# Kernel tuning notes

Hardware: AMD Instinct MI355X
Metric: run time of the kernel (lower is better)

## Reference

```python
import jax, jax.numpy as jnp
import numpy as np

N_NODES = 50000
N_EDGES = 800000
C_IN = 128
C_OUT = 64
C_HID = 2 * C_OUT  # 128


def setup_inputs() -> dict:
    key = jax.random.key(0)
    ks = jax.random.split(key, 8)
    x = jax.random.normal(ks[0], (N_NODES, C_IN), dtype=jnp.float32)
    edge_index = jax.random.randint(ks[1], (2, N_EDGES), 0, N_NODES, dtype=jnp.int64)
    s1 = 1.0 / np.sqrt(C_IN)
    s2 = 1.0 / np.sqrt(C_HID)
    s3 = 1.0 / np.sqrt(C_OUT)
    W1 = jax.random.uniform(ks[2], (C_IN, C_HID), jnp.float32, -s1, s1)
    b1 = jnp.zeros((C_HID,), jnp.float32)
    W2 = jax.random.uniform(ks[3], (C_HID, C_OUT), jnp.float32, -s2, s2)
    b2 = jnp.zeros((C_OUT,), jnp.float32)
    Wb = jax.random.uniform(ks[4], (1, C_OUT, C_OUT), jnp.float32, -s3, s3)
    bb = jax.random.uniform(ks[5], (1,), jnp.float32, -s3, s3)
    return {"x": x, "edge_index": edge_index, "W1": W1, "b1": b1,
            "W2": W2, "b2": b2, "Wb": Wb, "bb": bb}


def gcn_conv(x, W, b, src, dst, n_nodes):
    # PyG GCNConv: h = x @ W; add self-loops; symmetric normalization D^-1/2 (A+I) D^-1/2.
    h = x @ W  # [N, F]
    ones = jnp.ones((src.shape[0],), h.dtype)
    deg = jax.ops.segment_sum(ones, dst, num_segments=n_nodes) + 1.0  # +1 for self-loop
    dinv = jax.lax.rsqrt(deg)
    norm = dinv[src] * dinv[dst]  # [E]
    msgs = h[src] * norm[:, None]  # [E, F]
    agg = jax.ops.segment_sum(msgs, dst, num_segments=n_nodes)
    # self-loop contribution: norm_ii = 1/deg_i
    agg = agg + h * (1.0 / deg)[:, None]
    return agg + b


def reference(x, edge_index, W1, b1, W2, b2, Wb, bb):
    src = edge_index[0]
    dst = edge_index[1]
    n = x.shape[0]
    # encode
    h = jax.nn.relu(gcn_conv(x, W1, b1, src, dst, n))
    z = gcn_conv(h, W2, b2, src, dst, n)  # [N, C_OUT]
    # decode: bilinear on (z[src], z[dst]) -> sigmoid
    zs = z[src]  # [E, C_OUT]
    zd = z[dst]  # [E, C_OUT]
    logits = jnp.einsum('ec,ocd,ed->eo', zs, Wb, zd) + bb  # [E, 1]
    return jax.nn.sigmoid(logits)
```

## Files before the change

kernel.cpp:

```cpp
#include <hip/hip_runtime.h>
#include <hip/hip_bf16.h>


#define N_NODES 50000
#define BSH 7
#define BSZ 128
#define NBUCK ((N_NODES + BSZ - 1) / BSZ)
#define EPB 4096
#define CAP 3072
#define DSPLIT 4

typedef unsigned int u32;
typedef unsigned short u16;
typedef unsigned long long u64;

typedef __attribute__((ext_vector_type(8))) short bf16x8;
typedef __attribute__((ext_vector_type(4))) float f32x4;
union frag_u { bf16x8 f; u32 u[4]; uint4 v; };

__device__ __forceinline__ float bflo(u32 u) { return __uint_as_float(u << 16); }
__device__ __forceinline__ float bfhi(u32 u) { return __uint_as_float(u & 0xffff0000u); }
__device__ __forceinline__ u32 f2bf(float f) {
    u32 b = __float_as_uint(f);
    return (b + 0x7fffu + ((b >> 16) & 1u)) >> 16;
}
__device__ __forceinline__ u32 pack2(float a, float b) { return f2bf(a) | (f2bf(b) << 16); }

__global__ __launch_bounds__(256) void gemm1_scatter(
        const float* __restrict__ X, const float* __restrict__ W,
        u16* __restrict__ O, int n_rows, int gblk,
        const int* __restrict__ src, const int* __restrict__ dst,
        int* __restrict__ bcur, u64* __restrict__ pair, int E) {
    constexpr int K = 128, NOUT = 128;
    constexpr int KP = K + 8;
    constexpr int NT = NOUT / 16;
    constexpr int KS = K / 32;
    __shared__ __align__(16) char smem[NOUT * KP * 2 * sizeof(u16)];
    int t = threadIdx.x;

    if ((int)blockIdx.x < gblk) {
        u16* Wt_hi = (u16*)smem;
        u16* Wt_lo = Wt_hi + NOUT * KP;
        for (int i4 = t; i4 < K * NOUT / 4; i4 += 256) {
            int k = (i4 * 4) / NOUT;
            int n0 = (i4 * 4) % NOUT;
            float4 w4 = *(const float4*)&W[(size_t)k * NOUT + n0];
            float wv[4] = {w4.x, w4.y, w4.z, w4.w};
#pragma unroll
            for (int q = 0; q < 4; q++) {
                u32 hi = f2bf(wv[q]);
                u32 lo = f2bf(wv[q] - bflo(hi));
                Wt_hi[(n0 + q) * KP + k] = (u16)hi;
                Wt_lo[(n0 + q) * KP + k] = (u16)lo;
            }
        }
        __syncthreads();

        int wave = t >> 6;
        int lane = t & 63;
        int m16 = lane & 15;
        int quad = lane >> 4;
        int row0 = blockIdx.x * 128 + wave * 32;

        f32x4 acc[2][NT] = {};
        for (int ks = 0; ks < KS; ks++) {
            frag_u a_hi[2], a_lo[2];
#pragma unroll
            for (int mt = 0; mt < 2; mt++) {
                int row = row0 + mt * 16 + m16;
                row = row < n_rows ? row : n_rows - 1;
                const float* Xp = X + (size_t)row * K + ks * 32 + quad * 8;
                float4 x0 = *(const float4*)Xp;
                float4 x1 = *(const float4*)(Xp + 4);
                float xv[8] = {x0.x, x0.y, x0.z, x0.w, x1.x, x1.y, x1.z, x1.w};
#pragma unroll
                for (int p = 0; p < 4; p++) {
                    u32 h0 = f2bf(xv[2 * p]), h1 = f2bf(xv[2 * p + 1]);
                    a_hi[mt].u[p] = h0 | (h1 << 16);
                    a_lo[mt].u[p] = pack2(xv[2 * p] - bflo(h0), xv[2 * p + 1] - bflo(h1));
                }
            }
#pragma unroll
            for (int nt = 0; nt < NT; nt++) {
                int n = nt * 16 + m16;
                frag_u b_hi, b_lo;
                b_hi.v = *(const uint4*)&Wt_hi[n * KP + ks * 32 + quad * 8];
                b_lo.v = *(const uint4*)&Wt_lo[n * KP + ks * 32 + quad * 8];
#pragma unroll
                for (int mt = 0; mt < 2; mt++) {
                    acc[mt][nt] = __builtin_amdgcn_mfma_f32_16x16x32_bf16(a_hi[mt].f, b_hi.f, acc[mt][nt], 0, 0, 0);
                    acc[mt][nt] = __builtin_amdgcn_mfma_f32_16x16x32_bf16(a_hi[mt].f, b_lo.f, acc[mt][nt], 0, 0, 0);
                    acc[mt][nt] = __builtin_amdgcn_mfma_f32_16x16x32_bf16(a_lo[mt].f, b_hi.f, acc[mt][nt], 0, 0, 0);
                }
            }
        }
#pragma unroll
        for (int mt = 0; mt < 2; mt++)
#pragma unroll
            for (int nt = 0; nt < NT; nt++)
#pragma unroll
                for (int r = 0; r < 4; r++) {
                    int row = row0 + mt * 16 + quad * 4 + r;
                    if (row < n_rows)
                        O[(size_t)row * NOUT + nt * 16 + m16] = (u16)f2bf(acc[mt][nt][r]);
                }
    } else {
        int* hist = (int*)smem;
        for (int i = t; i < NBUCK; i += 256) hist[i] = 0;
        __syncthreads();
        int base = ((int)blockIdx.x - gblk) * EPB;
        int s_[16], d_[16];
#pragma unroll
        for (int it = 0; it < 16; it++) {
            int e = base + it * 256 + t;
            if (e < E) {
                s_[it] = src[e];
                d_[it] = dst[e];
                atomicAdd(&hist[d_[it] >> BSH], 1);
            } else {
                d_[it] = -1;
            }
        }
        __syncthreads();
        for (int b = t; b < NBUCK; b += 256) {
            int c = hist[b];
            hist[b] = c ? (b * CAP + atomicAdd(&bcur[b], c)) : 0;
        }
        __syncthreads();
#pragma unroll
        for (int it = 0; it < 16; it++) {
            if (d_[it] >= 0) {
                int b = d_[it] >> BSH;
                int off = atomicAdd(&hist[b], 1);
                int e = base + it * 256 + t;
                pair[off] = (u64)((u32)s_[it] | ((u32)(d_[it] & (BSZ - 1)) << 16))
                          | ((u64)(u32)e << 32);
            }
        }
    }
}

__global__ __launch_bounds__(256) void bucket_sort(const u64* __restrict__ pair,
                                                   const int* __restrict__ bcur,
                                                   int* __restrict__ row_ptr,
                                                   int* __restrict__ col,
                                                   float* __restrict__ dinv,
                                                   float* __restrict__ inv, int n, int E) {
    __shared__ int ssum[256];
    __shared__ int cnt[BSZ];
    __shared__ int scn[BSZ];
    __shared__ int cur[BSZ];
    int t = threadIdx.x;
    int base = blockIdx.x << BSH;
    int nn = min(BSZ, n - base);
    int accp = 0;
    for (int i = t; i < (int)blockIdx.x; i += 256) accp += bcur[i];
    ssum[t] = accp;
    __syncthreads();
    for (int s = 128; s > 0; s >>= 1) {
        if (t < s) ssum[t] += ssum[t + s];
        __syncthreads();
    }
    int b0 = ssum[0];
    int cntE = bcur[blockIdx.x];
    int p0 = blockIdx.x * CAP;
    if (t < BSZ) cnt[t] = 0;
    __syncthreads();
    for (int j = t; j < cntE; j += 256)
        atomicAdd(&cnt[(int)((pair[p0 + j] >> 16) & (BSZ - 1))], 1);
    __syncthreads();
    if (t < BSZ) scn[t] = cnt[t];
    __syncthreads();
    for (int off = 1; off < BSZ; off <<= 1) {
        int a = (t < BSZ && t >= off) ? scn[t - off] : 0;
        __syncthreads();
        if (t < BSZ) scn[t] += a;
        __syncthreads();
    }
    if (t < nn) {
        int excl = b0 + scn[t] - cnt[t];
        row_ptr[base + t] = excl;
        cur[t] = excl;
        float d = (float)cnt[t] + 1.0f;
        dinv[base + t] = rsqrtf(d);
        inv[base + t] = 1.0f / d;
    }
    if (t == 0 && blockIdx.x == NBUCK - 1) row_ptr[n] = E;
    __syncthreads();
    for (int j = t; j < cntE; j += 256) {
        u64 p = pair[p0 + j];
        int ln = (int)((p >> 16) & (BSZ - 1));
        int pos = atomicAdd(&cur[ln], 1);
        col[pos] = (int)(p & 0xffffu);
    }
}

template <int K, int NOUT>
__global__ __launch_bounds__(256) void gemm_mfma_bf(const u16* __restrict__ Xv,
                                                    const float* __restrict__ W,
                                                    u16* __restrict__ O, int n_rows) {
    constexpr int KP = K + 8;
    constexpr int NT = NOUT / 16;
    constexpr int KS = K / 32;
    __shared__ __align__(16) u16 Wt_hi[NOUT * KP];
    __shared__ __align__(16) u16 Wt_lo[NOUT * KP];
    int t = threadIdx.x;
    for (int i4 = t; i4 < K * NOUT / 4; i4 += 256) {
        int k = (i4 * 4) / NOUT;
        int n0 = (i4 * 4) % NOUT;
        float4 w4 = *(const float4*)&W[(size_t)k * NOUT + n0];
        float wv[4] = {w4.x, w4.y, w4.z, w4.w};
#pragma unroll
        for (int q = 0; q < 4; q++) {
            u32 hi = f2bf(wv[q]);
            u32 lo = f2bf(wv[q] - bflo(hi));
            Wt_hi[(n0 + q) * KP + k] = (u16)hi;
            Wt_lo[(n0 + q) * KP + k] = (u16)lo;
        }
    }
    __syncthreads();

    int wave = t >> 6;
    int lane = t & 63;
    int m16 = lane & 15;
    int quad = lane >> 4;
    int row0 = blockIdx.x * 128 + wave * 32;

    f32x4 acc[2][NT] = {};
    for (int ks = 0; ks < KS; ks++) {
        frag_u a_hi[2];
#pragma unroll
        for (int mt = 0; mt < 2; mt++) {
            int row = row0 + mt * 16 + m16;
            row = row < n_rows ? row : n_rows - 1;
            a_hi[mt].v = *(const uint4*)(Xv + (size_t)row * K + ks * 32 + quad * 8);
        }
#pragma unroll
        for (int nt = 0; nt < NT; nt++) {
            int n = nt * 16 + m16;
            frag_u b_hi, b_lo;
            b_hi.v = *(const uint4*)&Wt_hi[n * KP + ks * 32 + quad * 8];
            b_lo.v = *(const uint4*)&Wt_lo[n * KP + ks * 32 + quad * 8];
#pragma unroll
            for (int mt = 0; mt < 2; mt++) {
                acc[mt][nt] = __builtin_amdgcn_mfma_f32_16x16x32_bf16(a_hi[mt].f, b_hi.f, acc[mt][nt], 0, 0, 0);
                acc[mt][nt] = __builtin_amdgcn_mfma_f32_16x16x32_bf16(a_hi[mt].f, b_lo.f, acc[mt][nt], 0, 0, 0);
            }
        }
    }
#pragma unroll
    for (int mt = 0; mt < 2; mt++)
#pragma unroll
        for (int nt = 0; nt < NT; nt++)
#pragma unroll
            for (int r = 0; r < 4; r++) {
                int row = row0 + mt * 16 + quad * 4 + r;
                if (row < n_rows)
                    O[(size_t)row * NOUT + nt * 16 + m16] = (u16)f2bf(acc[mt][nt][r]);
            }
}

template <int C, bool RELU>
__global__ __launch_bounds__(256) void agg_pull(const u16* __restrict__ H,
                                                const int* __restrict__ row_ptr,
                                                const int* __restrict__ col,
                                                const float* __restrict__ dinv,
                                                const float* __restrict__ inv,
                                                const float* __restrict__ b,
                                                u16* __restrict__ O, int n) {
    constexpr int TPN = C / 8;
    const uint4* Hv = (const uint4*)H;
    int tid = blockIdx.x * 256 + threadIdx.x;
    int node = tid / TPN;
    if (node >= n) return;
    int part = tid % TPN;
    int c8 = part * 8;
    float dn = dinv[node];
    float iv = inv[node];
    float acc[8];
    {
        uint4 h = Hv[(size_t)node * TPN + part];
        acc[0] = bflo(h.x) * iv + b[c8 + 0];
        acc[1] = bfhi(h.x) * iv + b[c8 + 1];
        acc[2] = bflo(h.y) * iv + b[c8 + 2];
        acc[3] = bfhi(h.y) * iv + b[c8 + 3];
        acc[4] = bflo(h.z) * iv + b[c8 + 4];
        acc[5] = bfhi(h.z) * iv + b[c8 + 5];
        acc[6] = bflo(h.w) * iv + b[c8 + 6];
        acc[7] = bfhi(h.w) * iv + b[c8 + 7];
    }
    int j = row_ptr[node];
    int end = row_ptr[node + 1];
    for (; j + 7 < end; j += 8) {
        int s0 = col[j],     s1 = col[j + 1], s2 = col[j + 2], s3 = col[j + 3];
        int s4 = col[j + 4], s5 = col[j + 5], s6 = col[j + 6], s7 = col[j + 7];
        float n0 = dn * dinv[s0], n1 = dn * dinv[s1];
        float n2 = dn * dinv[s2], n3 = dn * dinv[s3];
        float n4 = dn * dinv[s4], n5 = dn * dinv[s5];
        float n6 = dn * dinv[s6], n7 = dn * dinv[s7];
        uint4 v0 = Hv[(size_t)s0 * TPN + part];
        uint4 v1 = Hv[(size_t)s1 * TPN + part];
        uint4 v2 = Hv[(size_t)s2 * TPN + part];
        uint4 v3 = Hv[(size_t)s3 * TPN + part];
        uint4 v4 = Hv[(size_t)s4 * TPN + part];
        uint4 v5 = Hv[(size_t)s5 * TPN + part];
        uint4 v6 = Hv[(size_t)s6 * TPN + part];
        uint4 v7 = Hv[(size_t)s7 * TPN + part];
        acc[0] += bflo(v0.x) * n0 + bflo(v1.x) * n1 + bflo(v2.x) * n2 + bflo(v3.x) * n3;
        acc[1] += bfhi(v0.x) * n0 + bfhi(v1.x) * n1 + bfhi(v2.x) * n2 + bfhi(v3.x) * n3;
        acc[2] += bflo(v0.y) * n0 + bflo(v1.y) * n1 + bflo(v2.y) * n2 + bflo(v3.y) * n3;
        acc[3] += bfhi(v0.y) * n0 + bfhi(v1.y) * n1 + bfhi(v2.y) * n2 + bfhi(v3.y) * n3;
        acc[4] += bflo(v0.z) * n0 + bflo(v1.z) * n1 + bflo(v2.z) * n2 + bflo(v3.z) * n3;
        acc[5] += bfhi(v0.z) * n0 + bfhi(v1.z) * n1 + bfhi(v2.z) * n2 + bfhi(v3.z) * n3;
        acc[6] += bflo(v0.w) * n0 + bflo(v1.w) * n1 + bflo(v2.w) * n2 + bflo(v3.w) * n3;
        acc[7] += bfhi(v0.w) * n0 + bfhi(v1.w) * n1 + bfhi(v2.w) * n2 + bfhi(v3.w) * n3;
        acc[0] += bflo(v4.x) * n4 + bflo(v5.x) * n5 + bflo(v6.x) * n6 + bflo(v7.x) * n7;
        acc[1] += bfhi(v4.x) * n4 + bfhi(v5.x) * n5 + bfhi(v6.x) * n6 + bfhi(v7.x) * n7;
        acc[2] += bflo(v4.y) * n4 + bflo(v5.y) * n5 + bflo(v6.y) * n6 + bflo(v7.y) * n7;
        acc[3] += bfhi(v4.y) * n4 + bfhi(v5.y) * n5 + bfhi(v6.y) * n6 + bfhi(v7.y) * n7;
        acc[4] += bflo(v4.z) * n4 + bflo(v5.z) * n5 + bflo(v6.z) * n6 + bflo(v7.z) * n7;
        acc[5] += bfhi(v4.z) * n4 + bfhi(v5.z) * n5 + bfhi(v6.z) * n6 + bfhi(v7.z) * n7;
        acc[6] += bflo(v4.w) * n4 + bflo(v5.w) * n5 + bflo(v6.w) * n6 + bflo(v7.w) * n7;
        acc[7] += bfhi(v4.w) * n4 + bfhi(v5.w) * n5 + bfhi(v6.w) * n6 + bfhi(v7.w) * n7;
    }
    for (; j + 3 < end; j += 4) {
        int s0 = col[j], s1 = col[j + 1], s2 = col[j + 2], s3 = col[j + 3];
        float n0 = dn * dinv[s0], n1 = dn * dinv[s1];
        float n2 = dn * dinv[s2], n3 = dn * dinv[s3];
        uint4 v0 = Hv[(size_t)s0 * TPN + part];
        uint4 v1 = Hv[(size_t)s1 * TPN + part];
        uint4 v2 = Hv[(size_t)s2 * TPN + part];
        uint4 v3 = Hv[(size_t)s3 * TPN + part];
        acc[0] += bflo(v0.x) * n0 + bflo(v1.x) * n1 + bflo(v2.x) * n2 + bflo(v3.x) * n3;
        acc[1] += bfhi(v0.x) * n0 + bfhi(v1.x) * n1 + bfhi(v2.x) * n2 + bfhi(v3.x) * n3;
        acc[2] += bflo(v0.y) * n0 + bflo(v1.y) * n1 + bflo(v2.y) * n2 + bflo(v3.y) * n3;
        acc[3] += bfhi(v0.y) * n0 + bfhi(v1.y) * n1 + bfhi(v2.y) * n2 + bfhi(v3.y) * n3;
        acc[4] += bflo(v0.z) * n0 + bflo(v1.z) * n1 + bflo(v2.z) * n2 + bflo(v3.z) * n3;
        acc[5] += bfhi(v0.z) * n0 + bfhi(v1.z) * n1 + bfhi(v2.z) * n2 + bfhi(v3.z) * n3;
        acc[6] += bflo(v0.w) * n0 + bflo(v1.w) * n1 + bflo(v2.w) * n2 + bflo(v3.w) * n3;
        acc[7] += bfhi(v0.w) * n0 + bfhi(v1.w) * n1 + bfhi(v2.w) * n2 + bfhi(v3.w) * n3;
    }
    for (; j < end; j++) {
        int s = col[j];
        float nm = dn * dinv[s];
        uint4 v = Hv[(size_t)s * TPN + part];
        acc[0] += bflo(v.x) * nm; acc[1] += bfhi(v.x) * nm;
        acc[2] += bflo(v.y) * nm; acc[3] += bfhi(v.y) * nm;
        acc[4] += bflo(v.z) * nm; acc[5] += bfhi(v.z) * nm;
        acc[6] += bflo(v.w) * nm; acc[7] += bfhi(v.w) * nm;
    }
    if (RELU) {
#pragma unroll
        for (int i = 0; i < 8; i++) acc[i] = fmaxf(acc[i], 0.f);
    }
    uint4 o;
    o.x = pack2(acc[0], acc[1]);
    o.y = pack2(acc[2], acc[3]);
    o.z = pack2(acc[4], acc[5]);
    o.w = pack2(acc[6], acc[7]);
    ((uint4*)O)[(size_t)node * TPN + part] = o;
}

__global__ __launch_bounds__(256) void decode_fused(const u16* __restrict__ Z,
                                                    const float* __restrict__ Wb,
                                                    const u64* __restrict__ pair,
                                                    const int* __restrict__ bcur,
                                                    const float* __restrict__ bb,
                                                    float* __restrict__ out, int n) {
    constexpr int K = 64, NOUT = 64;
    constexpr int KP = K + 8;
    constexpr int QP = 72;
    __shared__ __align__(16) u16 Wt_hi[NOUT * KP];
    __shared__ __align__(16) u16 Wt_lo[NOUT * KP];
    __shared__ __align__(16) u16 Qs[BSZ * QP];
    int t = threadIdx.x;
    int bucket = blockIdx.x / DSPLIT;
    int part = blockIdx.x % DSPLIT;
    int base = bucket << BSH;

    for (int i4 = t; i4 < K * NOUT / 4; i4 += 256) {
        int nn_ = (i4 * 4) / K;
        int k0 = (i4 * 4) % K;
        float4 w4 = *(const float4*)&Wb[(size_t)nn_ * K + k0];
        float wv[4] = {w4.x, w4.y, w4.z, w4.w};
#pragma unroll
        for (int q = 0; q < 4; q++) {
            u32 hi = f2bf(wv[q]);
            u32 lo = f2bf(wv[q] - bflo(hi));
            Wt_hi[nn_ * KP + k0 + q] = (u16)hi;
            Wt_lo[nn_ * KP + k0 + q] = (u16)lo;
        }
    }
    __syncthreads();

    {
        int wave = t >> 6;
        int lane = t & 63;
        int m16 = lane & 15;
        int quad = lane >> 4;
        int row0 = wave * 32;
        f32x4 acc[2][4] = {};
        for (int ks = 0; ks < 2; ks++) {
            frag_u a[2];
#pragma unroll
            for (int mt = 0; mt < 2; mt++) {
                int node = base + row0 + mt * 16 + m16;
                node = node < n ? node : n - 1;
                a[mt].v = *(const uint4*)(Z + (size_t)node * K + ks * 32 + quad * 8);
            }
#pragma unroll
            for (int nt = 0; nt < 4; nt++) {
                int nc = nt * 16 + m16;
                frag_u b_hi, b_lo;
                b_hi.v = *(const uint4*)&Wt_hi[nc * KP + ks * 32 + quad * 8];
                b_lo.v = *(const uint4*)&Wt_lo[nc * KP + ks * 32 + quad * 8];
#pragma unroll
                for (int mt = 0; mt < 2; mt++) {
                    acc[mt][nt] = __builtin_amdgcn_mfma_f32_16x16x32_bf16(a[mt].f, b_hi.f, acc[mt][nt], 0, 0, 0);
                    acc[mt][nt] = __builtin_amdgcn_mfma_f32_16x16x32_bf16(a[mt].f, b_lo.f, acc[mt][nt], 0, 0, 0);
                }
            }
        }
#pragma unroll
        for (int mt = 0; mt < 2; mt++)
#pragma unroll
            for (int nt = 0; nt < 4; nt++)
#pragma unroll
                for (int r = 0; r < 4; r++) {
                    int rl = row0 + mt * 16 + quad * 4 + r;
                    Qs[rl * QP + nt * 16 + m16] = (u16)f2bf(acc[mt][nt][r]);
                }
    }
    __syncthreads();

    const uint4* Zv = (const uint4*)Z;
    int cntE = bcur[bucket];
    int p0 = bucket * CAP;
    int chunk = (cntE + DSPLIT - 1) / DSPLIT;
    int s0 = part * chunk;
    int s1 = min(s0 + chunk, cntE);
    float bbv = bb[0];
    int lane8 = t & 7;
    int grp = t >> 3;
    for (int j = s0 + grp * 2; j < s1; j += 64) {
        u64 pA = pair[p0 + j];
        bool has2 = (j + 1) < s1;
        u64 pB = has2 ? pair[p0 + j + 1] : pA;
        int sA = (int)(pA & 0xffffu);
        int sB = (int)(pB & 0xffffu);
        int locA = (int)((pA >> 16) & (BSZ - 1));
        int locB = (int)((pB >> 16) & (BSZ - 1));
        uint4 zA = Zv[(size_t)sA * 8 + lane8];
        uint4 zB = Zv[(size_t)sB * 8 + lane8];
        uint4 qA = *(const uint4*)&Qs[locA * QP + lane8 * 8];
        uint4 qB = *(const uint4*)&Qs[locB * QP + lane8 * 8];
        float dA = bflo(zA.x) * bflo(qA.x) + bfhi(zA.x) * bfhi(qA.x)
                 + bflo(zA.y) * bflo(qA.y) + bfhi(zA.y) * bfhi(qA.y)
                 + bflo(zA.z) * bflo(qA.z) + bfhi(zA.z) * bfhi(qA.z)
                 + bflo(zA.w) * bflo(qA.w) + bfhi(zA.w) * bfhi(qA.w);
        float dB = bflo(zB.x) * bflo(qB.x) + bfhi(zB.x) * bfhi(qB.x)
                 + bflo(zB.y) * bflo(qB.y) + bfhi(zB.y) * bfhi(qB.y)
                 + bflo(zB.z) * bflo(qB.z) + bfhi(zB.z) * bfhi(qB.z)
                 + bflo(zB.w) * bflo(qB.w) + bfhi(zB.w) * bfhi(qB.w);
        dA += __shfl_down(dA, 4, 8);
        dA += __shfl_down(dA, 2, 8);
        dA += __shfl_down(dA, 1, 8);
        dB += __shfl_down(dB, 4, 8);
        dB += __shfl_down(dB, 2, 8);
        dB += __shfl_down(dB, 1, 8);
        if (lane8 == 0) {
            out[(int)(pA >> 32)] = 1.0f / (1.0f + expf(-(dA + bbv)));
            if (has2) out[(int)(pB >> 32)] = 1.0f / (1.0f + expf(-(dB + bbv)));
        }
    }
}

extern "C" void kernel_launch(void* const* d_in, const int* in_sizes, int n_in,
                              void* d_out, int out_size, void* d_ws, size_t ws_size,
                              hipStream_t stream) {
    const float* x  = (const float*)d_in[0];
    const int*   ei = (const int*)d_in[1];
    const float* W1 = (const float*)d_in[2];
    const float* b1 = (const float*)d_in[3];
    const float* W2 = (const float*)d_in[4];
    const float* b2 = (const float*)d_in[5];
    const float* Wb = (const float*)d_in[6];
    const float* bb = (const float*)d_in[7];
    float* out = (float*)d_out;

    const int N = N_NODES;
    const int E = in_sizes[1] / 2;
    const int* src = ei;
    const int* dst = ei + E;
    const int GBLK = (N + 127) / 128;
    const int SBLK = (E + EPB - 1) / EPB;

    char* w = (char*)d_ws;
    int*   bcur    = (int*)w;   w += (size_t)512 * 4;
    int*   row_ptr = (int*)w;   w += (size_t)(N + 1) * 4;
    int*   col     = (int*)w;   w += (size_t)E * 4;
    w = (char*)(((size_t)w + 15) & ~(size_t)15);
    u64*   pair    = (u64*)w;   w += (size_t)NBUCK * CAP * 8;
    float* dinv    = (float*)w; w += (size_t)N * 4;
    float* inv     = (float*)w; w += (size_t)N * 4;
    w = (char*)(((size_t)w + 15) & ~(size_t)15);
    u16* bufA = (u16*)w;        w += (size_t)N * 128 * 2;
    u16* bufB = (u16*)w;        w += (size_t)N * 128 * 2;
    u16* bufC = (u16*)w;

    u16* H1 = bufA;
    u16* h1 = bufB;
    u16* H2 = bufA;
    u16* Z  = bufC;

    hipMemsetAsync(bcur, 0, 512 * 4, stream);
    gemm1_scatter<<<GBLK + SBLK, 256, 0, stream>>>(x, W1, H1, N, GBLK,
                                                   src, dst, bcur, pair, E);
    bucket_sort<<<NBUCK, 256, 0, stream>>>(pair, bcur, row_ptr, col, dinv, inv, N, E);

    agg_pull<128, true><<<((size_t)N * 16 + 255) / 256, 256, 0, stream>>>(
        H1, row_ptr, col, dinv, inv, b1, h1, N);

    gemm_mfma_bf<128, 64><<<GBLK, 256, 0, stream>>>(h1, W2, H2, N);
    agg_pull<64, false><<<((size_t)N * 8 + 255) / 256, 256, 0, stream>>>(
        H2, row_ptr, col, dinv, inv, b2, Z, N);

    decode_fused<<<NBUCK * DSPLIT, 256, 0, stream>>>(Z, Wb, pair, bcur, bb, out, N);
}
```

Measured before the change: 229.5 us.

## Pre-sort bucket edges by source block in shared memory for locality

Inside bucket_sort, each bucket's edge pairs are staged into shared memory and counting-sorted by the high bits of the source index before the CSR columns are written. The sorted pairs are also written back to global memory. The aim is to improve the locality of the later gathers that read neighbor rows during aggregation, and to reuse the shared copy instead of re-reading pairs from global memory. In exchange the kernel uses 48KB more shared memory and adds extra scan and sort passes.

```diff
diff --git a/kernel.cpp b/kernel.cpp
--- a/kernel.cpp
+++ b/kernel.cpp
@@ -140,21 +140,26 @@
     }
 }
 
-__global__ __launch_bounds__(256) void bucket_sort(const u64* __restrict__ pair,
+__global__ __launch_bounds__(256) void bucket_sort(u64* __restrict__ pair,
                                                    const int* __restrict__ bcur,
                                                    int* __restrict__ row_ptr,
                                                    int* __restrict__ col,
                                                    float* __restrict__ dinv,
                                                    float* __restrict__ inv, int n, int E) {
+    __shared__ u64 prA[CAP];
+    __shared__ u64 prB[CAP];
     __shared__ int ssum[256];
+    __shared__ int histA[512];
+    __shared__ int scA[512];
     __shared__ int cnt[BSZ];
     __shared__ int scn[BSZ];
     __shared__ int cur[BSZ];
     int t = threadIdx.x;
-    int base = blockIdx.x << BSH;
+    int bucket = blockIdx.x;
+    int base = bucket << BSH;
     int nn = min(BSZ, n - base);
     int accp = 0;
-    for (int i = t; i < (int)blockIdx.x; i += 256) accp += bcur[i];
+    for (int i = t; i < bucket; i += 256) accp += bcur[i];
     ssum[t] = accp;
     __syncthreads();
     for (int s = 128; s > 0; s >>= 1) {
@@ -162,12 +167,45 @@
         __syncthreads();
     }
     int b0 = ssum[0];
-    int cntE = bcur[blockIdx.x];
-    int p0 = blockIdx.x * CAP;
+    int cntE = bcur[bucket];
+    int p0 = bucket * CAP;
+
+    histA[t] = 0;
+    histA[t + 256] = 0;
+    __syncthreads();
+    for (int j = t; j < cntE; j += 256) {
+        u64 p = pair[p0 + j];
+        prA[j] = p;
+        atomicAdd(&histA[(int)(p & 0xffffu) >> BSH], 1);
+    }
+    __syncthreads();
+    int h0 = histA[t], h1 = histA[t + 256];
+    scA[t] = h0;
+    scA[t + 256] = h1;
+    __syncthreads();
+    for (int off = 1; off < 512; off <<= 1) {
+        int a0 = (t >= off) ? scA[t - off] : 0;
+        int a1 = (t + 256 >= off) ? scA[t + 256 - off] : 0;
+        __syncthreads();
+        scA[t] += a0;
+        scA[t + 256] += a1;
+        __syncthreads();
+    }
+    histA[t] = scA[t] - h0;
+    histA[t + 256] = scA[t + 256] - h1;
+    __syncthreads();
+    for (int j = t; j < cntE; j += 256) {
+        u64 p = prA[j];
+        int pos = atomicAdd(&histA[(int)(p & 0xffffu) >> BSH], 1);
+        prB[pos] = p;
+    }
+    __syncthreads();
+    for (int j = t; j < cntE; j += 256) pair[p0 + j] = prB[j];
+
     if (t < BSZ) cnt[t] = 0;
     __syncthreads();
     for (int j = t; j < cntE; j += 256)
-        atomicAdd(&cnt[(int)((pair[p0 + j] >> 16) & (BSZ - 1))], 1);
+        atomicAdd(&cnt[(int)((prB[j] >> 16) & (BSZ - 1))], 1);
     __syncthreads();
     if (t < BSZ) scn[t] = cnt[t];
     __syncthreads();
@@ -185,10 +223,10 @@
         dinv[base + t] = rsqrtf(d);
         inv[base + t] = 1.0f / d;
     }
-    if (t == 0 && blockIdx.x == NBUCK - 1) row_ptr[n] = E;
+    if (t == 0 && bucket == NBUCK - 1) row_ptr[n] = E;
     __syncthreads();
     for (int j = t; j < cntE; j += 256) {
-        u64 p = pair[p0 + j];
+        u64 p = prB[j];
         int ln = (int)((p >> 16) & (BSZ - 1));
         int pos = atomicAdd(&cur[ln], 1);
         col[pos] = (int)(p & 0xffffu);
```

Result: faster. 223.7 us (-2.5%).
